# Kernel optimization log

Hardware: AMD Instinct MI355X
Metric: run time of the kernel (lower is better)

## Reference

```python
import jax, jax.numpy as jnp
import numpy as np

B = 16          # graphs per batch (equal-sized, contiguous)
N_PER = 16384   # nodes per graph
N = B * N_PER   # 262144 total nodes
E = 524288      # total edges
D_IN = 128
D_OUT = 128
RATIO = 0.5
K = int(N_PER * RATIO)  # nodes kept per graph by TopKPooling
NEG_SLOPE = 0.01        # F.leaky_relu default


def setup_inputs() -> dict:
    key = jax.random.key(0)
    ks = jax.random.split(key, 7)
    x = jax.random.normal(ks[0], (N, D_IN), jnp.float32)
    # edges constrained within each graph so per-graph pooling is meaningful
    e_per = E // B
    off = (jnp.arange(B, dtype=jnp.int32) * N_PER)[:, None]
    src = jax.random.randint(ks[1], (B, e_per), 0, N_PER, dtype=jnp.int32) + off
    dst = jax.random.randint(ks[2], (B, e_per), 0, N_PER, dtype=jnp.int32) + off
    edge_index = jnp.stack([src.reshape(-1), dst.reshape(-1)], axis=0)
    edge_weight = jax.random.uniform(ks[3], (E,), jnp.float32)
    batch = jnp.repeat(jnp.arange(B, dtype=jnp.int32), N_PER)
    conv_weight = jax.random.normal(ks[4], (D_IN, D_OUT), jnp.float32) / np.sqrt(D_IN)
    conv_bias = jnp.zeros((D_OUT,), jnp.float32)
    pool_weight = jax.random.normal(ks[5], (D_OUT,), jnp.float32)
    return {"x": x, "edge_index": edge_index, "edge_weight": edge_weight,
            "batch": batch, "conv_weight": conv_weight, "conv_bias": conv_bias,
            "pool_weight": pool_weight}


def reference(x, edge_index, edge_weight, batch, conv_weight, conv_bias, pool_weight):
    # Dropout is identity in eval mode (p=0.0).
    row, col = edge_index[0], edge_index[1]

    # ---- GCNConv: gcn_norm with added self-loops (fill_value=1) ----
    loop = jnp.arange(N, dtype=row.dtype)
    row_sl = jnp.concatenate([row, loop])
    col_sl = jnp.concatenate([col, loop])
    w_sl = jnp.concatenate([edge_weight, jnp.ones((N,), edge_weight.dtype)])
    deg = jax.ops.segment_sum(w_sl, col_sl, num_segments=N)          # in-degree at targets
    dinv = jnp.where(deg > 0, jax.lax.rsqrt(deg), 0.0)
    norm = dinv[row_sl] * w_sl * dinv[col_sl]                        # [E+N]

    xw = x @ conv_weight                                             # [N, D_OUT]
    msgs = norm[:, None] * xw[row_sl]                                # gather at sources
    h = jax.ops.segment_sum(msgs, col_sl, num_segments=N) + conv_bias  # scatter-add at targets
    h = jax.nn.leaky_relu(h, NEG_SLOPE)

    # ---- TopKPooling: score = tanh(x . w / ||w||), keep top K per graph ----
    score = jnp.tanh((h @ pool_weight) / jnp.linalg.norm(pool_weight))  # [N]
    _, idx = jax.lax.top_k(score.reshape(B, N_PER), K)                  # [B, K] local idx
    perm = (idx + (jnp.arange(B, dtype=idx.dtype) * N_PER)[:, None]).reshape(-1)  # [B*K]

    x_out = h[perm] * score[perm][:, None]                              # gate kept nodes
    batch_new = batch[perm]

    # ---- filter_adj: relabel, keep edges whose both endpoints survive ----
    mapping = jnp.full((N,), -1, dtype=row.dtype).at[perm].set(
        jnp.arange(B * K, dtype=row.dtype))
    r2, c2 = mapping[row], mapping[col]
    valid = (r2 >= 0) & (c2 >= 0)
    edge_index_new = jnp.where(valid, jnp.stack([r2, c2], axis=0), 0)   # padded (static shape)
    edge_weight_new = jnp.where(valid, edge_weight, 0.0)
    return x_out, edge_index_new, edge_weight_new, batch_new
```

## Files before the change

kernel.cpp:

```cpp
#include <hip/hip_runtime.h>
#include <math.h>

#define N_NODES 262144
#define N_EDGES 524288
#define NB      16
#define N_PER   16384
#define KKEEP   8192
#define DIM     128
#define NEG_SLOPE 0.01f
#define CHUNK   2048

#define X_OUT   0
#define X_EI    16777216
#define X_EW    17825792
#define X_BATCH 18350080

__device__ __forceinline__ unsigned long long pack_key(float sc, int localIdx) {
    unsigned int u = __float_as_uint(sc);
    u = (u & 0x80000000u) ? ~u : (u | 0x80000000u);
    unsigned int inv = ~u;
    return ((unsigned long long)inv << 32) | (unsigned int)localIdx;
}

__global__ void k_init(float* deg, int* count, int* mapping, const float* pw, float* normPw) {
    int n = blockIdx.x * 256 + threadIdx.x;
    if (n < N_NODES) { deg[n] = 1.0f; count[n] = 0; mapping[n] = -1; }
    if (n == 0) {
        float s = 0.f;
        for (int i = 0; i < DIM; i++) s += pw[i] * pw[i];
        normPw[0] = sqrtf(s);
    }
}

__global__ void k_deg(const int* col, const float* w, float* deg, int* count) {
    int e = blockIdx.x * 256 + threadIdx.x;
    if (e >= N_EDGES) return;
    int c = col[e];
    atomicAdd(&deg[c], w[e]);
    atomicAdd(&count[c], 1);
}

__global__ void k_scan1(const int* count, int* offs, int* blockSums) {
    __shared__ int s[2048];
    int base = blockIdx.x * 2048;
    int t = threadIdx.x;
    s[t]        = count[base + t];
    s[t + 1024] = count[base + t + 1024];
    __syncthreads();
    for (int off = 1; off < 2048; off <<= 1) {
        int a0 = (t >= off)        ? s[t - off]        : 0;
        int a1 = (t + 1024 >= off) ? s[t + 1024 - off] : 0;
        __syncthreads();
        s[t]        += a0;
        s[t + 1024] += a1;
        __syncthreads();
    }
    offs[base + t]        = s[t]        - count[base + t];
    offs[base + t + 1024] = s[t + 1024] - count[base + t + 1024];
    if (t == 0) blockSums[blockIdx.x] = s[2047];
}

__global__ void k_scan2(int* blockSums, int* offs) {
    if (threadIdx.x == 0) {
        int run = 0;
        for (int b = 0; b < 128; b++) { int v = blockSums[b]; blockSums[b] = run; run += v; }
        offs[N_NODES] = run;
    }
}

__global__ void k_fixup(int* offs, int* count, float* deg, const int* blockSums) {
    int n = blockIdx.x * 256 + threadIdx.x;
    if (n >= N_NODES) return;
    offs[n] += blockSums[n >> 11];
    count[n] = 0;
    float d = deg[n];
    deg[n] = (d > 0.f) ? (1.0f / sqrtf(d)) : 0.f;
}

__global__ void k_scatter(const int* row, const int* col, const float* w, const float* dinv,
                          const int* offs, int* cursor, int* ssrc, float* scoef) {
    int e = blockIdx.x * 256 + threadIdx.x;
    if (e >= N_EDGES) return;
    int r = row[e], c = col[e];
    int pos = atomicAdd(&cursor[c], 1);
    int slot = offs[c] + pos;
    ssrc[slot]  = r;
    scoef[slot] = (dinv[r] * w[e]) * dinv[c];
}

__global__ void k_aggregate(const float* x, const float* dinv, const int* offs,
                            const int* ssrc, const float* scoef, float* agg) {
    int g = blockIdx.x * 256 + threadIdx.x;
    int node = g >> 5, d = g & 31;
    const float4* x4 = (const float4*)x;
    float4 acc = make_float4(0.f, 0.f, 0.f, 0.f);
    int s = offs[node], e = offs[node + 1];
    for (int j = s; j < e; j++) {
        int   src = ssrc[j];
        float cf  = scoef[j];
        float4 v = x4[(size_t)src * 32 + d];
        acc.x += cf * v.x; acc.y += cf * v.y; acc.z += cf * v.z; acc.w += cf * v.w;
    }
    float di = dinv[node];
    float cf = di * di;
    float4 v = x4[(size_t)node * 32 + d];
    acc.x += cf * v.x; acc.y += cf * v.y; acc.z += cf * v.z; acc.w += cf * v.w;
    ((float4*)agg)[(size_t)node * 32 + d] = acc;
}

__global__ __launch_bounds__(256, 2) void k_gemm(float* hio, const float* Wg,
                                                 const float* bias, const float* pw,
                                                 const float* normPw, float* score) {
    __shared__ __align__(16) float sW[32 * 128];
    __shared__ __align__(16) float sA[32 * 128];
    int tid = threadIdx.x;
    int cx = tid & 15;
    int ry = tid >> 4;
    int row0 = blockIdx.x * 128;

    float acc[8][8];
#pragma unroll
    for (int r = 0; r < 8; r++)
#pragma unroll
        for (int c = 0; c < 8; c++) acc[r][c] = 0.f;

    for (int k0 = 0; k0 < DIM; k0 += 32) {
#pragma unroll
        for (int i = 0; i < 4; i++) {
            int f = tid + i * 256;
            int kk = f >> 5, j4 = f & 31;
            *(float4*)(sW + kk * 128 + j4 * 4) =
                *(const float4*)(Wg + (size_t)(k0 + kk) * 128 + j4 * 4);
        }
#pragma unroll
        for (int i = 0; i < 4; i++) {
            int f = tid + i * 256;
            int r = f >> 3, k4 = f & 7;
            float4 v = *(const float4*)(hio + (size_t)(row0 + r) * 128 + k0 + k4 * 4);
            int rs = r ^ (k4 * 8);
            sA[(k4 * 4 + 0) * 128 + rs] = v.x;
            sA[(k4 * 4 + 1) * 128 + rs] = v.y;
            sA[(k4 * 4 + 2) * 128 + rs] = v.z;
            sA[(k4 * 4 + 3) * 128 + rs] = v.w;
        }
        __syncthreads();
#pragma unroll
        for (int kk = 0; kk < 32; kk++) {
            const float* ap = sA + kk * 128 + ((8 * ry) ^ ((kk >> 2) * 8));
            float4 a0 = *(const float4*)(ap);
            float4 a1 = *(const float4*)(ap + 4);
            float4 w0 = *(const float4*)(sW + kk * 128 + 8 * cx);
            float4 w1 = *(const float4*)(sW + kk * 128 + 8 * cx + 4);
            float av[8] = {a0.x, a0.y, a0.z, a0.w, a1.x, a1.y, a1.z, a1.w};
            float wv[8] = {w0.x, w0.y, w0.z, w0.w, w1.x, w1.y, w1.z, w1.w};
#pragma unroll
            for (int r = 0; r < 8; r++)
#pragma unroll
                for (int c = 0; c < 8; c++) acc[r][c] += av[r] * wv[c];
        }
        __syncthreads();
    }

    float bv[8], pv[8];
#pragma unroll
    for (int c = 0; c < 8; c++) { bv[c] = bias[8 * cx + c]; pv[c] = pw[8 * cx + c]; }
    float nrm = normPw[0];

#pragma unroll
    for (int r = 0; r < 8; r++) {
        int row = row0 + 8 * ry + r;
        float hv[8];
        float p = 0.f;
#pragma unroll
        for (int c = 0; c < 8; c++) {
            float v = acc[r][c] + bv[c];
            v = (v >= 0.f) ? v : NEG_SLOPE * v;
            hv[c] = v;
            p += v * pv[c];
        }
        float4 o0 = make_float4(hv[0], hv[1], hv[2], hv[3]);
        float4 o1 = make_float4(hv[4], hv[5], hv[6], hv[7]);
        *(float4*)(hio + (size_t)row * 128 + 8 * cx)     = o0;
        *(float4*)(hio + (size_t)row * 128 + 8 * cx + 4) = o1;
#pragma unroll
        for (int m = 1; m < 16; m <<= 1) p += __shfl_xor(p, m, 64);
        if (cx == 0) score[row] = tanhf(p / nrm);
    }
}

__global__ __launch_bounds__(1024) void k_sortchunks(const float* score,
                                                     unsigned long long* keys) {
    __shared__ unsigned long long a[CHUNK];
    int base = blockIdx.x * CHUNK;
    int t = threadIdx.x;
#pragma unroll
    for (int i = 0; i < CHUNK / 1024; i++) {
        int p = t + i * 1024;
        int node = base + p;
        a[p] = pack_key(score[node], node & (N_PER - 1));
    }
    __syncthreads();
    for (int k = 2; k <= CHUNK; k <<= 1) {
        for (int j = k >> 1; j > 0; j >>= 1) {
#pragma unroll
            for (int q = 0; q < CHUNK / 2048; q++) {
                int tt = t + q * 1024;
                int i = ((tt & ~(j - 1)) << 1) | (tt & (j - 1));
                int l = i | j;
                bool asc = ((i & k) == 0);
                unsigned long long x = a[i], y = a[l];
                if ((x > y) == asc) { a[i] = y; a[l] = x; }
            }
            __syncthreads();
        }
    }
#pragma unroll
    for (int i = 0; i < CHUNK / 1024; i++) {
        int p = t + i * 1024;
        keys[base + p] = a[p];
    }
}

__global__ void k_rank(const float* score, const unsigned long long* keys,
                       int* perm, int* mapping, float* out) {
    int n = blockIdx.x * 256 + threadIdx.x;
    if (n >= N_NODES) return;
    int g = n >> 14;
    unsigned long long key = pack_key(score[n], n & (N_PER - 1));
    const unsigned long long* gb = keys + ((size_t)g << 14);
    int r = 0;
#pragma unroll
    for (int c = 0; c < N_PER / CHUNK; c++) {
        const unsigned long long* ch = gb + c * CHUNK;
        int lo = 0, hi = CHUNK;
        while (lo < hi) {
            int mid = (lo + hi) >> 1;
            if (ch[mid] < key) lo = mid + 1; else hi = mid;
        }
        r += lo;
    }
    if (r < KKEEP) {
        int i = (g << 13) + r;
        perm[i] = n;
        mapping[n] = i;
        out[X_BATCH + i] = (float)g;
    }
}

__global__ void k_gate(const float* h, const float* score, const int* perm, float* out) {
    int g = blockIdx.x * 256 + threadIdx.x;
    int i = g >> 5, d = g & 31;
    int node = perm[i];
    float sc = score[node];
    float4 v = ((const float4*)h)[(size_t)node * 32 + d];
    v.x *= sc; v.y *= sc; v.z *= sc; v.w *= sc;
    ((float4*)(out + X_OUT))[(size_t)i * 32 + d] = v;
}

__global__ void k_edges(const int* row, const int* col, const float* w,
                        const int* mapping, float* out) {
    int e = blockIdx.x * 256 + threadIdx.x;
    if (e >= N_EDGES) return;
    int mr = mapping[row[e]], mc = mapping[col[e]];
    bool valid = (mr >= 0) && (mc >= 0);
    out[X_EI + e]           = valid ? (float)mr : 0.f;
    out[X_EI + N_EDGES + e] = valid ? (float)mc : 0.f;
    out[X_EW + e]           = valid ? w[e] : 0.f;
}

extern "C" void kernel_launch(void* const* d_in, const int* in_sizes, int n_in,
                              void* d_out, int out_size, void* d_ws, size_t ws_size,
                              hipStream_t stream) {
    const float* x     = (const float*)d_in[0];
    const int*   ei    = (const int*)d_in[1];
    const float* ew    = (const float*)d_in[2];
    const float* Wc    = (const float*)d_in[4];
    const float* bias  = (const float*)d_in[5];
    const float* pw    = (const float*)d_in[6];
    float* out = (float*)d_out;

    const int* rowp = ei;
    const int* colp = ei + N_EDGES;

    char* wsb = (char*)d_ws;
    float* agg     = (float*)(wsb);
    float* dinv    = (float*)(wsb + 134217728);
    int*   count   = (int*)  (wsb + 135266304);
    int*   offs    = (int*)  (wsb + 136314880);
    int*   ssrc    = (int*)  (wsb + 137363712);
    float* scoef   = (float*)(wsb + 139460864);
    float* score   = (float*)(wsb + 141557760);
    unsigned long long* keys = (unsigned long long*)(wsb + 142606336);
    int*   perm    = (int*)  (wsb + 144703488);
    int*   mapping = (int*)  (wsb + 145227776);
    int*   blockSums = (int*)(wsb + 146276352);
    float* normPw  = (float*)(wsb + 146277376);

    k_init   <<<N_NODES / 256, 256, 0, stream>>>(dinv, count, mapping, pw, normPw);
    k_deg    <<<N_EDGES / 256, 256, 0, stream>>>(colp, ew, dinv, count);
    k_scan1  <<<128, 1024, 0, stream>>>(count, offs, blockSums);
    k_scan2  <<<1, 64, 0, stream>>>(blockSums, offs);
    k_fixup  <<<N_NODES / 256, 256, 0, stream>>>(offs, count, dinv, blockSums);
    k_scatter<<<N_EDGES / 256, 256, 0, stream>>>(rowp, colp, ew, dinv, offs, count, ssrc, scoef);
    k_aggregate<<<(N_NODES * 32) / 256, 256, 0, stream>>>(x, dinv, offs, ssrc, scoef, agg);
    k_gemm   <<<N_NODES / 128, 256, 0, stream>>>(agg, Wc, bias, pw, normPw, score);
    k_sortchunks<<<N_NODES / CHUNK, 1024, 0, stream>>>(score, keys);
    k_rank   <<<N_NODES / 256, 256, 0, stream>>>(score, keys, perm, mapping, out);
    k_gate   <<<(NB * KKEEP * 32) / 256, 256, 0, stream>>>(agg, score, perm, out);
    k_edges  <<<N_EDGES / 256, 256, 0, stream>>>(rowp, colp, ew, mapping, out);
}
```

Measured before the change: 551.2 us.

## Pack edge src/coef into int2 and remap aggregate blocks per XCD by graph

Edge source index and coefficient are stored interleaved as one int2, so the aggregate loop makes one 8-byte load per edge instead of two separate 4-byte loads. Aggregate blocks are also remapped so that each of the 8 XCDs handles two whole graphs. Because edges stay inside a graph, each XCD's gathered x rows then fall in a 16 MB window, which should improve L2 hit rates. The int2 buffer uses the old ssrc+scoef region, 4 MB at offset 137363712, and fits before score.

```diff
diff --git a/kernel.cpp b/kernel.cpp
--- a/kernel.cpp
+++ b/kernel.cpp
@@ -78,27 +78,33 @@
 }
 
 __global__ void k_scatter(const int* row, const int* col, const float* w, const float* dinv,
-                          const int* offs, int* cursor, int* ssrc, float* scoef) {
+                          const int* offs, int* cursor, int2* sedge) {
     int e = blockIdx.x * 256 + threadIdx.x;
     if (e >= N_EDGES) return;
     int r = row[e], c = col[e];
     int pos = atomicAdd(&cursor[c], 1);
     int slot = offs[c] + pos;
-    ssrc[slot]  = r;
-    scoef[slot] = (dinv[r] * w[e]) * dinv[c];
+    float coef = (dinv[r] * w[e]) * dinv[c];
+    sedge[slot] = make_int2(r, __float_as_int(coef));
 }
 
 __global__ void k_aggregate(const float* x, const float* dinv, const int* offs,
-                            const int* ssrc, const float* scoef, float* agg) {
-    int g = blockIdx.x * 256 + threadIdx.x;
-    int node = g >> 5, d = g & 31;
+                            const int2* sedge, float* agg) {
+    int blk = blockIdx.x;
+    int xcd = blk & 7;
+    int local = blk >> 3;
+    int g = xcd * 2 + (local >> 11);
+    int blkInGraph = local & 2047;
+    int node = g * N_PER + blkInGraph * 8 + (threadIdx.x >> 5);
+    int d = threadIdx.x & 31;
+
     const float4* x4 = (const float4*)x;
     float4 acc = make_float4(0.f, 0.f, 0.f, 0.f);
     int s = offs[node], e = offs[node + 1];
     for (int j = s; j < e; j++) {
-        int   src = ssrc[j];
-        float cf  = scoef[j];
-        float4 v = x4[(size_t)src * 32 + d];
+        int2 ed = sedge[j];
+        float cf = __int_as_float(ed.y);
+        float4 v = x4[(size_t)ed.x * 32 + d];
         acc.x += cf * v.x; acc.y += cf * v.y; acc.z += cf * v.z; acc.w += cf * v.w;
     }
     float di = dinv[node];
@@ -287,8 +293,7 @@
     float* dinv    = (float*)(wsb + 134217728);
     int*   count   = (int*)  (wsb + 135266304);
     int*   offs    = (int*)  (wsb + 136314880);
-    int*   ssrc    = (int*)  (wsb + 137363712);
-    float* scoef   = (float*)(wsb + 139460864);
+    int2*  sedge   = (int2*) (wsb + 137363712);
     float* score   = (float*)(wsb + 141557760);
     unsigned long long* keys = (unsigned long long*)(wsb + 142606336);
     int*   perm    = (int*)  (wsb + 144703488);
@@ -301,8 +306,8 @@
     k_scan1  <<<128, 1024, 0, stream>>>(count, offs, blockSums);
     k_scan2  <<<1, 64, 0, stream>>>(blockSums, offs);
     k_fixup  <<<N_NODES / 256, 256, 0, stream>>>(offs, count, dinv, blockSums);
-    k_scatter<<<N_EDGES / 256, 256, 0, stream>>>(rowp, colp, ew, dinv, offs, count, ssrc, scoef);
-    k_aggregate<<<(N_NODES * 32) / 256, 256, 0, stream>>>(x, dinv, offs, ssrc, scoef, agg);
+    k_scatter<<<N_EDGES / 256, 256, 0, stream>>>(rowp, colp, ew, dinv, offs, count, sedge);
+    k_aggregate<<<(N_NODES * 32) / 256, 256, 0, stream>>>(x, dinv, offs, sedge, agg);
     k_gemm   <<<N_NODES / 128, 256, 0, stream>>>(agg, Wc, bias, pw, normPw, score);
     k_sortchunks<<<N_NODES / CHUNK, 1024, 0, stream>>>(score, keys);
     k_rank   <<<N_NODES / 256, 256, 0, stream>>>(score, keys, perm, mapping, out);
```

Result: no change. 560.1 us (+1.6%).
